# Kernel optimization log

Hardware: AMD Instinct MI355X
Metric: run time of the kernel (lower is better)

The kernel has to match this reference:

```python
import jax, jax.numpy as jnp
import numpy as np

B, T, N, K1, H, C = 2, 8, 5000, 17, 4, 16  # K1 = self + 16 neighbors
N_OUT = (C + 1) // 2


def setup_inputs() -> dict:
    key = jax.random.key(0)
    kf, kn, km = jax.random.split(key, 3)
    # small scale so exp(-||Mdf||^2) stays in a numerically interesting range
    features = jax.random.normal(kf, (B, T, N, H, C), dtype=jnp.float32) * 0.1
    nearest = jax.random.randint(kn, (N, K1), 0, N, dtype=jnp.int32)
    nearest = nearest.at[:, 0].set(jnp.arange(N, dtype=jnp.int32))  # col 0 = self
    drop = (jax.random.uniform(km, (N, K1)) < 0.05) & (jnp.arange(K1)[None, :] > 0)
    nearest = jnp.where(drop, jnp.int32(-1), nearest)
    # faithful parameter init: [I | 0] blocks scaled by Q1_init / Q2_init, diag(M_init)
    q_form = jnp.zeros((H, N_OUT, C), dtype=jnp.float32).at[:, :, :N_OUT].set(jnp.eye(N_OUT, dtype=jnp.float32))
    multiQ1 = q_form * 1.2
    multiQ2 = q_form * 0.8
    multiM = jnp.broadcast_to(jnp.eye(C, dtype=jnp.float32), (H, C, C)) * 1.5
    return {"features": features, "nearest_nodes": nearest,
            "multiQ1": multiQ1, "multiQ2": multiQ2, "multiM": multiM}


def reference(features, nearest_nodes, multiQ1, multiQ2, multiM):
    B_, T_, N_, H_, C_ = features.shape
    # pad row N_ is all-zeros; -1 sentinel indices are routed to it
    pad = jnp.concatenate([features, jnp.zeros_like(features[:, :, :1])], axis=2)  # (B,T,N+1,H,C)
    idx = jnp.where(nearest_nodes < 0, N_, nearest_nodes)  # (N, K1)

    # ---------------- undirected ----------------
    nbr = idx[:, 1:]                       # (N, K) neighbor indices (excl. self)
    fj = pad[:, :, nbr]                    # (B,T,N,K,H,C) gathered neighbor feats
    df = features[:, :, :, None] - fj      # (B,T,N,K,H,C)
    Mdf = jnp.einsum('hij,btnkhj->btnkhi', multiM, df)
    w = jnp.exp(-jnp.sum(Mdf * Mdf, axis=-1))              # (B,T,N,K,H)
    valid = (nearest_nodes[:, 1:] >= 0)[None, None, :, :, None]
    w = w * valid
    deg = jnp.sum(w, axis=3)                               # (B,T,N,H)
    pad_deg = jnp.concatenate([deg, jnp.zeros_like(deg[:, :, :1])], axis=2)
    deg_j = pad_deg[:, :, nbr]                             # (B,T,N,K,H)
    dmul = jnp.sqrt(deg[:, :, :, None] * deg_j)
    inv = jnp.where(dmul > 0, 1.0 / jnp.where(dmul > 0, dmul, 1.0), 0.0)
    u_w = w * inv                                          # (B,T,N,K,H)

    # ---------------- directed ----------------
    fi = pad[:, :-1, idx]                                  # (B,T-1,N,K1,H,C)
    Qi = jnp.einsum('hij,btnkhj->btnkhi', multiQ1, fi)     # (B,T-1,N,K1,H,n_out)
    Qj = jnp.einsum('hij,btnhj->btnhi', multiQ2, features[:, 1:])  # (B,T-1,N,H,n_out)
    wd = jnp.exp(-jnp.sum(Qi * Qj[:, :, :, None], axis=-1))        # (B,T-1,N,K1,H)
    wd = wd * (nearest_nodes >= 0)[None, None, :, :, None]
    in_deg = jnp.sum(wd, axis=3)                           # (B,T-1,N,H)
    inv_d = jnp.where(in_deg > 0, 1.0 / jnp.where(in_deg > 0, in_deg, 1.0), 0.0)
    d_w = wd * inv_d[:, :, :, None]                        # (B,T-1,N,K1,H)

    return (u_w, d_w)
```

## Files before the change

kernel.cpp:

```cpp
#include <hip/hip_runtime.h>
#include <cstdio>

#define BB 2
#define TT 8
#define NNODE 5000
#define KK1 17
#define HH 4
#define NT (BB*TT*NNODE)
#define NREST (BB*7*NNODE)
#define DEG_BLOCKS 10000
#define DW_BLOCKS 1094

typedef unsigned short u16;
typedef unsigned int u32;

__device__ __forceinline__ u16 f2bf(float x) {
  u32 u = __float_as_uint(x);
  u32 r = (u + 0x7fffu + ((u >> 16) & 1u)) >> 16;
  return (u16)r;
}
__device__ __forceinline__ float bfLo(u32 w){ return __uint_as_float(w << 16); }
__device__ __forceinline__ float bfHi(u32 w){ return __uint_as_float(w & 0xffff0000u); }

__device__ __forceinline__ float edge_e(uint4 A0, uint4 A1, uint4 B0, uint4 B1) {
  u32 aw[8] = {A0.x,A0.y,A0.z,A0.w,A1.x,A1.y,A1.z,A1.w};
  u32 bw[8] = {B0.x,B0.y,B0.z,B0.w,B1.x,B1.y,B1.z,B1.w};
  float dot = 0.f, si = 0.f, sj = 0.f;
#pragma unroll
  for (int r = 0; r < 8; ++r) {
    float al = bfLo(aw[r]), ah = bfHi(aw[r]);
    float bl = bfLo(bw[r]), bh = bfHi(bw[r]);
    dot = fmaf(al, bl, dot); dot = fmaf(ah, bh, dot);
    si  = fmaf(al, al, si);  si  = fmaf(ah, ah, si);
    sj  = fmaf(bl, bl, sj);  sj  = fmaf(bh, bh, sj);
  }
  return si + sj - 2.f*dot;
}

__global__ void __launch_bounds__(256) k_prep(
    const float* __restrict__ feat, const float* __restrict__ mm,
    const float* __restrict__ q1, const float* __restrict__ q2,
    u16* __restrict__ g, u16* __restrict__ a8, u16* __restrict__ b8) {
  const int lane = threadIdx.x & 63;
  const int h = lane >> 4, i = lane & 15;
  const int bid = blockIdx.x;
  const int x = bid & 7;
  const int local = (bid >> 3) * 4 + (threadIdx.x >> 6);
  const int mbase = x * 10000 + local * 10;
  float Mrow[16], Qrow[16];
  const float* qsrc = (i < 8) ? (q1 + (h*8 + i)*16) : (q2 + (h*8 + (i - 8))*16);
#pragma unroll
  for (int j = 0; j < 16; ++j) {
    Mrow[j] = mm[(h*16 + i)*16 + j];
    Qrow[j] = qsrc[j];
  }
#pragma unroll 2
  for (int l = 0; l < 10; ++l) {
    const int m = mbase + l;
    const float4* fp = reinterpret_cast<const float4*>(feat + (size_t)m*64 + h*16);
    float fv[16];
#pragma unroll
    for (int q = 0; q < 4; ++q) {
      float4 v = fp[q];
      fv[q*4+0] = v.x; fv[q*4+1] = v.y; fv[q*4+2] = v.z; fv[q*4+3] = v.w;
    }
    float accG = 0.f, accQ = 0.f;
#pragma unroll
    for (int j = 0; j < 16; ++j) {
      accG = fmaf(Mrow[j], fv[j], accG);
      accQ = fmaf(Qrow[j], fv[j], accQ);
    }
    g[(size_t)m*64 + lane] = f2bf(accG);
    if (i < 8) a8[(size_t)m*32 + h*8 + i] = f2bf(accQ);
    else       b8[(size_t)m*32 + h*8 + (i - 8)] = f2bf(accQ);
  }
}

__global__ void __launch_bounds__(256) k_degdw(
    const u16* __restrict__ g, const u16* __restrict__ a8, const u16* __restrict__ b8,
    const int* __restrict__ nn, float* __restrict__ deg,
    u16* __restrict__ wstage, float* __restrict__ dw) {
  __shared__ float lds[64*68];
  const int bid = blockIdx.x;
  if (bid < DEG_BLOCKS) {
    const int x = bid & 7;
    const int n = (bid >> 3)*4 + (threadIdx.x >> 6);
    const int lane = threadIdx.x & 63;
    const int k = lane >> 2, h = lane & 3;
    const int m0 = (2*x)*NNODE + n;
    const int m1 = m0 + NNODE;
    int jr = nn[n*KK1 + 1 + k];
    bool v = jr >= 0;
    int j = v ? jr : 0;
    const uint4* pi0 = reinterpret_cast<const uint4*>(g + (size_t)m0*64 + h*16);
    const uint4* pi1 = reinterpret_cast<const uint4*>(g + (size_t)m1*64 + h*16);
    const uint4* pj0 = reinterpret_cast<const uint4*>(g + (size_t)((2*x)*NNODE + j)*64 + h*16);
    const uint4* pj1 = reinterpret_cast<const uint4*>(g + (size_t)((2*x+1)*NNODE + j)*64 + h*16);
    uint4 A00 = pi0[0], A01 = pi0[1];
    uint4 A10 = pi1[0], A11 = pi1[1];
    uint4 B00 = pj0[0], B01 = pj0[1];
    uint4 B10 = pj1[0], B11 = pj1[1];
    float e0 = edge_e(A00, A01, B00, B01);
    float e1 = edge_e(A10, A11, B10, B11);
    float w0 = v ? __expf(-e0) : 0.f;
    float w1 = v ? __expf(-e1) : 0.f;
    const int soff = ((lane >> 3) << 4) + (lane & 7);
    wstage[(size_t)m0*128 + soff] = f2bf(w0);
    wstage[(size_t)m1*128 + soff] = f2bf(w1);
    float d0 = w0, d1 = w1;
    d0 += __shfl_xor(d0, 4);  d1 += __shfl_xor(d1, 4);
    d0 += __shfl_xor(d0, 8);  d1 += __shfl_xor(d1, 8);
    d0 += __shfl_xor(d0, 16); d1 += __shfl_xor(d1, 16);
    d0 += __shfl_xor(d0, 32); d1 += __shfl_xor(d1, 32);
    if (lane < 4) {
      deg[m0*4 + lane] = d0;
      deg[m1*4 + lane] = d1;
    }
  } else {
    const int wg = bid - DEG_BLOCKS;
    const int lr = threadIdx.x >> 2;
    const int h  = threadIdx.x & 3;
    const int lane = threadIdx.x & 63;
    const int qbase = lane & ~3;
    const int rest = wg*64 + lr;
    if (rest < NREST) {
      const int n = rest % NNODE;
      const int q2 = rest / NNODE;
      const int b = q2 / 7, t = q2 % 7;
      uint4 Bv = *reinterpret_cast<const uint4*>(b8 + ((size_t)((b*TT + t + 1)*NNODE + n))*32 + h*8);
      float bv[8] = {bfLo(Bv.x), bfHi(Bv.x), bfLo(Bv.y), bfHi(Bv.y),
                     bfLo(Bv.z), bfHi(Bv.z), bfLo(Bv.w), bfHi(Bv.w)};
      const int nbase = n*KK1;
      const int abase = (b*TT + t)*NNODE;
      int jvec[4];
      jvec[0] = nn[nbase + h + 0];
      jvec[1] = nn[nbase + h + 4];
      jvec[2] = nn[nbase + h + 8];
      jvec[3] = nn[nbase + h + 12];
      int j16 = nn[nbase + 16];
      float wk[17];
      float indeg = 0.f;
#pragma unroll
      for (int kk = 0; kk < 16; ++kk) {
        int jr = __shfl(jvec[kk >> 2], qbase + (kk & 3));
        bool valid = jr >= 0;
        int j = valid ? jr : 0;
        uint4 Av = *reinterpret_cast<const uint4*>(a8 + ((size_t)(abase + j))*32 + h*8);
        float dot = 0.f;
        dot = fmaf(bfLo(Av.x), bv[0], dot); dot = fmaf(bfHi(Av.x), bv[1], dot);
        dot = fmaf(bfLo(Av.y), bv[2], dot); dot = fmaf(bfHi(Av.y), bv[3], dot);
        dot = fmaf(bfLo(Av.z), bv[4], dot); dot = fmaf(bfHi(Av.z), bv[5], dot);
        dot = fmaf(bfLo(Av.w), bv[6], dot); dot = fmaf(bfHi(Av.w), bv[7], dot);
        float w = valid ? __expf(-dot) : 0.f;
        wk[kk] = w;
        indeg += w;
      }
      {
        bool valid = j16 >= 0;
        int j = valid ? j16 : 0;
        uint4 Av = *reinterpret_cast<const uint4*>(a8 + ((size_t)(abase + j))*32 + h*8);
        float dot = 0.f;
        dot = fmaf(bfLo(Av.x), bv[0], dot); dot = fmaf(bfHi(Av.x), bv[1], dot);
        dot = fmaf(bfLo(Av.y), bv[2], dot); dot = fmaf(bfHi(Av.y), bv[3], dot);
        dot = fmaf(bfLo(Av.z), bv[4], dot); dot = fmaf(bfHi(Av.z), bv[5], dot);
        dot = fmaf(bfLo(Av.w), bv[6], dot); dot = fmaf(bfHi(Av.w), bv[7], dot);
        float w = valid ? __expf(-dot) : 0.f;
        wk[16] = w;
        indeg += w;
      }
      float inv = (indeg > 0.f) ? (1.0f / indeg) : 0.f;
#pragma unroll
      for (int kk = 0; kk < KK1; ++kk) lds[lr*68 + kk*4 + h] = wk[kk] * inv;
    }
    __syncthreads();
    const int rows = NREST - wg*64;
    const int nchunks = (rows >= 64 ? 64 : rows) * 17;
    float4* obase = reinterpret_cast<float4*>(dw + (size_t)wg*4352);
    for (int c = threadIdx.x; c < nchunks; c += 256) {
      const int row = c / 17;
      const int col = (c % 17) * 4;
      obase[c] = *reinterpret_cast<const float4*>(&lds[row*68 + col]);
    }
  }
}

__global__ void __launch_bounds__(256) k_uw(
    const int* __restrict__ nn, const float* __restrict__ deg,
    float* __restrict__ uw) {
  const int bid = blockIdx.x;
  const int x = bid & 7, sub = bid >> 3;
  const int wg = (x < 4 ? x*313 : 4*313 + (x-4)*312) + sub;
  const int idx8 = (wg * 256 + threadIdx.x) * 8;
  const int m = idx8 >> 6;
  const int r8 = idx8 & 63;
  const int k0 = r8 >> 2;
  const int n = m % NNODE;
  const int btb = m - n;
  uint4 wv = *reinterpret_cast<const uint4*>(uw + idx8);
  int jr0 = nn[n*KK1 + 1 + k0];
  int jr1 = nn[n*KK1 + 2 + k0];
  float4 di = *reinterpret_cast<const float4*>(deg + (size_t)m*4);
  uint4 o0 = {0u,0u,0u,0u}, o1 = {0u,0u,0u,0u};
  if (jr0 >= 0) {
    float4 dj = *reinterpret_cast<const float4*>(deg + (size_t)(btb + jr0)*4);
    float w0 = bfLo(wv.x), w1 = bfHi(wv.x), w2 = bfLo(wv.y), w3 = bfHi(wv.y);
    float p0 = di.x*dj.x, p1 = di.y*dj.y, p2 = di.z*dj.z, p3 = di.w*dj.w;
    o0.x = __float_as_uint((w0 > 0.f && p0 > 0.f) ? w0 * rsqrtf(p0) : 0.f);
    o0.y = __float_as_uint((w1 > 0.f && p1 > 0.f) ? w1 * rsqrtf(p1) : 0.f);
    o0.z = __float_as_uint((w2 > 0.f && p2 > 0.f) ? w2 * rsqrtf(p2) : 0.f);
    o0.w = __float_as_uint((w3 > 0.f && p3 > 0.f) ? w3 * rsqrtf(p3) : 0.f);
  }
  if (jr1 >= 0) {
    float4 dj = *reinterpret_cast<const float4*>(deg + (size_t)(btb + jr1)*4);
    float w0 = bfLo(wv.z), w1 = bfHi(wv.z), w2 = bfLo(wv.w), w3 = bfHi(wv.w);
    float p0 = di.x*dj.x, p1 = di.y*dj.y, p2 = di.z*dj.z, p3 = di.w*dj.w;
    o1.x = __float_as_uint((w0 > 0.f && p0 > 0.f) ? w0 * rsqrtf(p0) : 0.f);
    o1.y = __float_as_uint((w1 > 0.f && p1 > 0.f) ? w1 * rsqrtf(p1) : 0.f);
    o1.z = __float_as_uint((w2 > 0.f && p2 > 0.f) ? w2 * rsqrtf(p2) : 0.f);
    o1.w = __float_as_uint((w3 > 0.f && p3 > 0.f) ? w3 * rsqrtf(p3) : 0.f);
  }
  uint4* ob = reinterpret_cast<uint4*>(uw + idx8);
  ob[0] = o0;
  ob[1] = o1;
}

extern "C" void kernel_launch(void* const* d_in, const int* in_sizes, int n_in,
                              void* d_out, int out_size, void* d_ws, size_t ws_size,
                              hipStream_t stream) {
  const float* feat = (const float*)d_in[0];
  const int*   nn   = (const int*)d_in[1];
  const float* q1   = (const float*)d_in[2];
  const float* q2   = (const float*)d_in[3];
  const float* mm   = (const float*)d_in[4];
  float* uw = (float*)d_out;
  float* dw = uw + (size_t)NT*64;

  const size_t G_BYTES  = (size_t)NT*64*2;
  const size_t A_BYTES  = (size_t)NT*32*2;
  const size_t DEG_BYTES= (size_t)NT*4*4;
  const size_t NEED = G_BYTES + 2*A_BYTES + DEG_BYTES;
  if (ws_size < NEED) {
    fprintf(stderr, "kernel_launch: ws_size %zu < needed %zu\n", ws_size, NEED);
    return;
  }
  u16*   g   = (u16*)d_ws;
  u16*   a8  = (u16*)((char*)d_ws + G_BYTES);
  u16*   b8  = (u16*)((char*)d_ws + G_BYTES + A_BYTES);
  float* deg = (float*)((char*)d_ws + G_BYTES + 2*A_BYTES);
  u16*   wstage = (u16*)uw;

  k_prep <<<2000, 256, 0, stream>>>(feat, mm, q1, q2, g, a8, b8);
  k_degdw<<<DEG_BLOCKS + DW_BLOCKS, 256, 0, stream>>>(g, a8, b8, nn, deg, wstage, dw);
  k_uw   <<<2500, 256, 0, stream>>>(nn, deg, uw);
}
```

Before: 62.19 us.

## Stage per-slice projected features in LDS for undirected edge weights

The projected features are re-laid out per (b,t,h) slice, and each slice (5000 nodes x 16 bf16) is loaded into 160KB of swizzled LDS. The neighbor gathers for the undirected weights then read from LDS instead of global memory. A transposed neighbor table is built in the prep kernel. The u_w normalization kernel loads the slice's degrees into LDS. The directed path is split into its own kernel, giving four launches instead of three. In exchange, each slice is reloaded by 4 blocks, only 256 blocks run with one block per CU because of the LDS size, and an extra weight staging buffer goes through global memory.

Measured after the change: 78.81 us. 1.27x slower.

```diff
diff --git a/kernel.cpp b/kernel.cpp
--- a/kernel.cpp
+++ b/kernel.cpp
@@ -1,52 +1,41 @@
 #include <hip/hip_runtime.h>
 #include <cstdio>
 
-#define BB 2
-#define TT 8
 #define NNODE 5000
 #define KK1 17
-#define HH 4
-#define NT (BB*TT*NNODE)
-#define NREST (BB*7*NNODE)
-#define DEG_BLOCKS 10000
-#define DW_BLOCKS 1094
+#define NT 80000
+#define NREST 70000
 
 typedef unsigned short u16;
 typedef unsigned int u32;
 
 __device__ __forceinline__ u16 f2bf(float x) {
   u32 u = __float_as_uint(x);
-  u32 r = (u + 0x7fffu + ((u >> 16) & 1u)) >> 16;
-  return (u16)r;
+  return (u16)((u + 0x7fffu + ((u >> 16) & 1u)) >> 16);
 }
 __device__ __forceinline__ float bfLo(u32 w){ return __uint_as_float(w << 16); }
 __device__ __forceinline__ float bfHi(u32 w){ return __uint_as_float(w & 0xffff0000u); }
-
-__device__ __forceinline__ float edge_e(uint4 A0, uint4 A1, uint4 B0, uint4 B1) {
-  u32 aw[8] = {A0.x,A0.y,A0.z,A0.w,A1.x,A1.y,A1.z,A1.w};
-  u32 bw[8] = {B0.x,B0.y,B0.z,B0.w,B1.x,B1.y,B1.z,B1.w};
-  float dot = 0.f, si = 0.f, sj = 0.f;
-#pragma unroll
-  for (int r = 0; r < 8; ++r) {
-    float al = bfLo(aw[r]), ah = bfHi(aw[r]);
-    float bl = bfLo(bw[r]), bh = bfHi(bw[r]);
-    dot = fmaf(al, bl, dot); dot = fmaf(ah, bh, dot);
-    si  = fmaf(al, al, si);  si  = fmaf(ah, ah, si);
-    sj  = fmaf(bl, bl, sj);  sj  = fmaf(bh, bh, sj);
-  }
-  return si + sj - 2.f*dot;
-}
 
 __global__ void __launch_bounds__(256) k_prep(
     const float* __restrict__ feat, const float* __restrict__ mm,
     const float* __restrict__ q1, const float* __restrict__ q2,
-    u16* __restrict__ g, u16* __restrict__ a8, u16* __restrict__ b8) {
+    const int* __restrict__ nn,
+    u16* __restrict__ gS, u16* __restrict__ a8, u16* __restrict__ b8,
+    int* __restrict__ nnT) {
+  const int bid = blockIdx.x;
+  if (bid >= 2000) {
+    const int i = (bid - 2000)*256 + threadIdx.x;
+    if (i < KK1*NNODE) {
+      const int k = i / NNODE;
+      const int n = i - k*NNODE;
+      nnT[i] = nn[n*KK1 + k];
+    }
+    return;
+  }
   const int lane = threadIdx.x & 63;
   const int h = lane >> 4, i = lane & 15;
-  const int bid = blockIdx.x;
   const int x = bid & 7;
-  const int local = (bid >> 3) * 4 + (threadIdx.x >> 6);
-  const int mbase = x * 10000 + local * 10;
+  const int mbase = x*10000 + (bid >> 3)*40 + (threadIdx.x >> 6);
   float Mrow[16], Qrow[16];
   const float* qsrc = (i < 8) ? (q1 + (h*8 + i)*16) : (q2 + (h*8 + (i - 8))*16);
 #pragma unroll
@@ -56,7 +45,9 @@
   }
 #pragma unroll 2
   for (int l = 0; l < 10; ++l) {
-    const int m = mbase + l;
+    const int m = mbase + l*4;
+    const int bt = m / NNODE;
+    const int n = m - bt*NNODE;
     const float4* fp = reinterpret_cast<const float4*>(feat + (size_t)m*64 + h*16);
     float fv[16];
 #pragma unroll
@@ -70,158 +61,181 @@
       accG = fmaf(Mrow[j], fv[j], accG);
       accQ = fmaf(Qrow[j], fv[j], accQ);
     }
-    g[(size_t)m*64 + lane] = f2bf(accG);
+    gS[((size_t)(bt*4 + h)*NNODE + n)*16 + i] = f2bf(accG);
     if (i < 8) a8[(size_t)m*32 + h*8 + i] = f2bf(accQ);
     else       b8[(size_t)m*32 + h*8 + (i - 8)] = f2bf(accQ);
   }
 }
 
-__global__ void __launch_bounds__(256) k_degdw(
-    const u16* __restrict__ g, const u16* __restrict__ a8, const u16* __restrict__ b8,
-    const int* __restrict__ nn, float* __restrict__ deg,
-    u16* __restrict__ wstage, float* __restrict__ dw) {
+__global__ void __launch_bounds__(256) k_w(
+    const u16* __restrict__ gS, const int* __restrict__ nnT,
+    float* __restrict__ degS, u16* __restrict__ wS) {
+  __shared__ u32 glds[40000];
+  const int bid = blockIdx.x;
+  const int sl = bid & 63;
+  const int chunk = bid >> 6;
+  const u32* gsrc = reinterpret_cast<const u32*>(gS) + (size_t)sl*NNODE*8;
+  for (int n = threadIdx.x; n < NNODE; n += 256) {
+    const uint4* rp = reinterpret_cast<const uint4*>(gsrc + n*8);
+    uint4 v0 = rp[0], v1 = rp[1];
+    u32 wv[8] = {v0.x, v0.y, v0.z, v0.w, v1.x, v1.y, v1.z, v1.w};
+    const int sw = (n >> 2) & 7;
+#pragma unroll
+    for (int c = 0; c < 8; ++c) glds[n*8 + (c ^ sw)] = wv[c];
+  }
+  __syncthreads();
+  for (int r = 0; r < 5; ++r) {
+    const int ns = r*256 + threadIdx.x;
+    if (ns >= 1250) continue;
+    const int n = chunk*1250 + ns;
+    float av[16];
+    float si = 0.f;
+    const int swn = (n >> 2) & 7;
+#pragma unroll
+    for (int c = 0; c < 8; ++c) {
+      u32 wv = glds[n*8 + (c ^ swn)];
+      float lo = bfLo(wv), hi = bfHi(wv);
+      av[2*c] = lo; av[2*c+1] = hi;
+      si = fmaf(lo, lo, si); si = fmaf(hi, hi, si);
+    }
+    float deg = 0.f;
+    u32 packed[8];
+#pragma unroll 4
+    for (int k = 0; k < 16; ++k) {
+      const int jr = nnT[(1 + k)*NNODE + n];
+      const int j = (jr >= 0) ? jr : 0;
+      const int swj = (j >> 2) & 7;
+      float dot = 0.f, sj = 0.f;
+#pragma unroll
+      for (int c = 0; c < 8; ++c) {
+        u32 wv = glds[j*8 + (c ^ swj)];
+        float lo = bfLo(wv), hi = bfHi(wv);
+        dot = fmaf(av[2*c], lo, dot); dot = fmaf(av[2*c+1], hi, dot);
+        sj = fmaf(lo, lo, sj); sj = fmaf(hi, hi, sj);
+      }
+      float e = si + sj - 2.f*dot;
+      float w = (jr >= 0) ? __expf(-e) : 0.f;
+      deg += w;
+      u16 wb = f2bf(w);
+      if (k & 1) packed[k >> 1] |= ((u32)wb) << 16;
+      else       packed[k >> 1] = (u32)wb;
+    }
+    degS[(size_t)sl*NNODE + n] = deg;
+    uint4* wp = reinterpret_cast<uint4*>(wS + ((size_t)sl*NNODE + n)*16);
+    wp[0] = make_uint4(packed[0], packed[1], packed[2], packed[3]);
+    wp[1] = make_uint4(packed[4], packed[5], packed[6], packed[7]);
+  }
+}
+
+__global__ void __launch_bounds__(256) k_uw3(
+    const u16* __restrict__ wS, const int* __restrict__ nnT,
+    const float* __restrict__ degS, float* __restrict__ uw) {
+  __shared__ float dl[4*NNODE];
+  const int bid = blockIdx.x;
+  const int bt = bid & 15;
+  const int chunk = bid >> 4;
+  for (int i = threadIdx.x; i < 4*NNODE; i += 256) dl[i] = degS[(size_t)bt*4*NNODE + i];
+  __syncthreads();
+  const u32* wsrc = reinterpret_cast<const u32*>(wS);
+  for (int r = 0; r < 10; ++r) {
+    const int item = r*256 + threadIdx.x;
+    const int nsub = item >> 3, kp = item & 7;
+    const int n = chunk*313 + nsub;
+    if (nsub >= 313 || n >= NNODE) continue;
+    const int j0r = nnT[(1 + 2*kp)*NNODE + n];
+    const int j1r = nnT[(2 + 2*kp)*NNODE + n];
+    const int j0 = (j0r >= 0) ? j0r : 0;
+    const int j1 = (j1r >= 0) ? j1r : 0;
+    u32 wv[4];
+#pragma unroll
+    for (int h = 0; h < 4; ++h) wv[h] = wsrc[((size_t)(bt*4 + h)*NNODE + n)*8 + kp];
+    float o0[4], o1[4];
+#pragma unroll
+    for (int h = 0; h < 4; ++h) {
+      const float di  = dl[h*NNODE + n];
+      const float dj0 = dl[h*NNODE + j0];
+      const float dj1 = dl[h*NNODE + j1];
+      const float w0 = bfLo(wv[h]), w1 = bfHi(wv[h]);
+      const float p0 = di*dj0, p1 = di*dj1;
+      o0[h] = (j0r >= 0 && w0 > 0.f && p0 > 0.f) ? w0*rsqrtf(p0) : 0.f;
+      o1[h] = (j1r >= 0 && w1 > 0.f && p1 > 0.f) ? w1*rsqrtf(p1) : 0.f;
+    }
+    float4* ob = reinterpret_cast<float4*>(uw + (((size_t)bt*NNODE + n)*16 + 2*kp)*4);
+    ob[0] = make_float4(o0[0], o0[1], o0[2], o0[3]);
+    ob[1] = make_float4(o1[0], o1[1], o1[2], o1[3]);
+  }
+}
+
+__global__ void __launch_bounds__(256) k_dw(
+    const u16* __restrict__ a8, const u16* __restrict__ b8,
+    const int* __restrict__ nn, float* __restrict__ dw) {
   __shared__ float lds[64*68];
   const int bid = blockIdx.x;
-  if (bid < DEG_BLOCKS) {
-    const int x = bid & 7;
-    const int n = (bid >> 3)*4 + (threadIdx.x >> 6);
-    const int lane = threadIdx.x & 63;
-    const int k = lane >> 2, h = lane & 3;
-    const int m0 = (2*x)*NNODE + n;
-    const int m1 = m0 + NNODE;
-    int jr = nn[n*KK1 + 1 + k];
-    bool v = jr >= 0;
-    int j = v ? jr : 0;
-    const uint4* pi0 = reinterpret_cast<const uint4*>(g + (size_t)m0*64 + h*16);
-    const uint4* pi1 = reinterpret_cast<const uint4*>(g + (size_t)m1*64 + h*16);
-    const uint4* pj0 = reinterpret_cast<const uint4*>(g + (size_t)((2*x)*NNODE + j)*64 + h*16);
-    const uint4* pj1 = reinterpret_cast<const uint4*>(g + (size_t)((2*x+1)*NNODE + j)*64 + h*16);
-    uint4 A00 = pi0[0], A01 = pi0[1];
-    uint4 A10 = pi1[0], A11 = pi1[1];
-    uint4 B00 = pj0[0], B01 = pj0[1];
-    uint4 B10 = pj1[0], B11 = pj1[1];
-    float e0 = edge_e(A00, A01, B00, B01);
-    float e1 = edge_e(A10, A11, B10, B11);
-    float w0 = v ? __expf(-e0) : 0.f;
-    float w1 = v ? __expf(-e1) : 0.f;
-    const int soff = ((lane >> 3) << 4) + (lane & 7);
-    wstage[(size_t)m0*128 + soff] = f2bf(w0);
-    wstage[(size_t)m1*128 + soff] = f2bf(w1);
-    float d0 = w0, d1 = w1;
-    d0 += __shfl_xor(d0, 4);  d1 += __shfl_xor(d1, 4);
-    d0 += __shfl_xor(d0, 8);  d1 += __shfl_xor(d1, 8);
-    d0 += __shfl_xor(d0, 16); d1 += __shfl_xor(d1, 16);
-    d0 += __shfl_xor(d0, 32); d1 += __shfl_xor(d1, 32);
-    if (lane < 4) {
-      deg[m0*4 + lane] = d0;
-      deg[m1*4 + lane] = d1;
-    }
-  } else {
-    const int wg = bid - DEG_BLOCKS;
-    const int lr = threadIdx.x >> 2;
-    const int h  = threadIdx.x & 3;
-    const int lane = threadIdx.x & 63;
-    const int qbase = lane & ~3;
-    const int rest = wg*64 + lr;
-    if (rest < NREST) {
-      const int n = rest % NNODE;
-      const int q2 = rest / NNODE;
-      const int b = q2 / 7, t = q2 % 7;
-      uint4 Bv = *reinterpret_cast<const uint4*>(b8 + ((size_t)((b*TT + t + 1)*NNODE + n))*32 + h*8);
-      float bv[8] = {bfLo(Bv.x), bfHi(Bv.x), bfLo(Bv.y), bfHi(Bv.y),
-                     bfLo(Bv.z), bfHi(Bv.z), bfLo(Bv.w), bfHi(Bv.w)};
-      const int nbase = n*KK1;
-      const int abase = (b*TT + t)*NNODE;
-      int jvec[4];
-      jvec[0] = nn[nbase + h + 0];
-      jvec[1] = nn[nbase + h + 4];
-      jvec[2] = nn[nbase + h + 8];
-      jvec[3] = nn[nbase + h + 12];
-      int j16 = nn[nbase + 16];
-      float wk[17];
-      float indeg = 0.f;
-#pragma unroll
-      for (int kk = 0; kk < 16; ++kk) {
-        int jr = __shfl(jvec[kk >> 2], qbase + (kk & 3));
-        bool valid = jr >= 0;
-        int j = valid ? jr : 0;
-        uint4 Av = *reinterpret_cast<const uint4*>(a8 + ((size_t)(abase + j))*32 + h*8);
-        float dot = 0.f;
-        dot = fmaf(bfLo(Av.x), bv[0], dot); dot = fmaf(bfHi(Av.x), bv[1], dot);
-        dot = fmaf(bfLo(Av.y), bv[2], dot); dot = fmaf(bfHi(Av.y), bv[3], dot);
-        dot = fmaf(bfLo(Av.z), bv[4], dot); dot = fmaf(bfHi(Av.z), bv[5], dot);
-        dot = fmaf(bfLo(Av.w), bv[6], dot); dot = fmaf(bfHi(Av.w), bv[7], dot);
-        float w = valid ? __expf(-dot) : 0.f;
-        wk[kk] = w;
-        indeg += w;
-      }
-      {
-        bool valid = j16 >= 0;
-        int j = valid ? j16 : 0;
-        uint4 Av = *reinterpret_cast<const uint4*>(a8 + ((size_t)(abase + j))*32 + h*8);
-        float dot = 0.f;
-        dot = fmaf(bfLo(Av.x), bv[0], dot); dot = fmaf(bfHi(Av.x), bv[1], dot);
-        dot = fmaf(bfLo(Av.y), bv[2], dot); dot = fmaf(bfHi(Av.y), bv[3], dot);
-        dot = fmaf(bfLo(Av.z), bv[4], dot); dot = fmaf(bfHi(Av.z), bv[5], dot);
-        dot = fmaf(bfLo(Av.w), bv[6], dot); dot = fmaf(bfHi(Av.w), bv[7], dot);
-        float w = valid ? __expf(-dot) : 0.f;
-        wk[16] = w;
-        indeg += w;
-      }
-      float inv = (indeg > 0.f) ? (1.0f / indeg) : 0.f;
-#pragma unroll
-      for (int kk = 0; kk < KK1; ++kk) lds[lr*68 + kk*4 + h] = wk[kk] * inv;
-    }
-    __syncthreads();
-    const int rows = NREST - wg*64;
-    const int nchunks = (rows >= 64 ? 64 : rows) * 17;
-    float4* obase = reinterpret_cast<float4*>(dw + (size_t)wg*4352);
-    for (int c = threadIdx.x; c < nchunks; c += 256) {
-      const int row = c / 17;
-      const int col = (c % 17) * 4;
-      obase[c] = *reinterpret_cast<const float4*>(&lds[row*68 + col]);
-    }
-  }
-}
-
-__global__ void __launch_bounds__(256) k_uw(
-    const int* __restrict__ nn, const float* __restrict__ deg,
-    float* __restrict__ uw) {
-  const int bid = blockIdx.x;
   const int x = bid & 7, sub = bid >> 3;
-  const int wg = (x < 4 ? x*313 : 4*313 + (x-4)*312) + sub;
-  const int idx8 = (wg * 256 + threadIdx.x) * 8;
-  const int m = idx8 >> 6;
-  const int r8 = idx8 & 63;
-  const int k0 = r8 >> 2;
-  const int n = m % NNODE;
-  const int btb = m - n;
-  uint4 wv = *reinterpret_cast<const uint4*>(uw + idx8);
-  int jr0 = nn[n*KK1 + 1 + k0];
-  int jr1 = nn[n*KK1 + 2 + k0];
-  float4 di = *reinterpret_cast<const float4*>(deg + (size_t)m*4);
-  uint4 o0 = {0u,0u,0u,0u}, o1 = {0u,0u,0u,0u};
-  if (jr0 >= 0) {
-    float4 dj = *reinterpret_cast<const float4*>(deg + (size_t)(btb + jr0)*4);
-    float w0 = bfLo(wv.x), w1 = bfHi(wv.x), w2 = bfLo(wv.y), w3 = bfHi(wv.y);
-    float p0 = di.x*dj.x, p1 = di.y*dj.y, p2 = di.z*dj.z, p3 = di.w*dj.w;
-    o0.x = __float_as_uint((w0 > 0.f && p0 > 0.f) ? w0 * rsqrtf(p0) : 0.f);
-    o0.y = __float_as_uint((w1 > 0.f && p1 > 0.f) ? w1 * rsqrtf(p1) : 0.f);
-    o0.z = __float_as_uint((w2 > 0.f && p2 > 0.f) ? w2 * rsqrtf(p2) : 0.f);
-    o0.w = __float_as_uint((w3 > 0.f && p3 > 0.f) ? w3 * rsqrtf(p3) : 0.f);
-  }
-  if (jr1 >= 0) {
-    float4 dj = *reinterpret_cast<const float4*>(deg + (size_t)(btb + jr1)*4);
-    float w0 = bfLo(wv.z), w1 = bfHi(wv.z), w2 = bfLo(wv.w), w3 = bfHi(wv.w);
-    float p0 = di.x*dj.x, p1 = di.y*dj.y, p2 = di.z*dj.z, p3 = di.w*dj.w;
-    o1.x = __float_as_uint((w0 > 0.f && p0 > 0.f) ? w0 * rsqrtf(p0) : 0.f);
-    o1.y = __float_as_uint((w1 > 0.f && p1 > 0.f) ? w1 * rsqrtf(p1) : 0.f);
-    o1.z = __float_as_uint((w2 > 0.f && p2 > 0.f) ? w2 * rsqrtf(p2) : 0.f);
-    o1.w = __float_as_uint((w3 > 0.f && p3 > 0.f) ? w3 * rsqrtf(p3) : 0.f);
-  }
-  uint4* ob = reinterpret_cast<uint4*>(uw + idx8);
-  ob[0] = o0;
-  ob[1] = o1;
+  const int wg = (x < 6 ? x*137 : 6*137 + (x-6)*136) + sub;
+  const int lr = threadIdx.x >> 2;
+  const int h  = threadIdx.x & 3;
+  const int lane = threadIdx.x & 63;
+  const int qbase = lane & ~3;
+  const int rest = wg*64 + lr;
+  if (rest < NREST) {
+    const int n = rest % NNODE;
+    const int q2 = rest / NNODE;
+    const int b = q2 / 7, t = q2 % 7;
+    uint4 Bv = *reinterpret_cast<const uint4*>(b8 + ((size_t)((b*8 + t + 1)*NNODE + n))*32 + h*8);
+    float bv[8] = {bfLo(Bv.x), bfHi(Bv.x), bfLo(Bv.y), bfHi(Bv.y),
+                   bfLo(Bv.z), bfHi(Bv.z), bfLo(Bv.w), bfHi(Bv.w)};
+    const int nbase = n*KK1;
+    const int abase = (b*8 + t)*NNODE;
+    int jvec[4];
+    jvec[0] = nn[nbase + h + 0];
+    jvec[1] = nn[nbase + h + 4];
+    jvec[2] = nn[nbase + h + 8];
+    jvec[3] = nn[nbase + h + 12];
+    int j16 = nn[nbase + 16];
+    float wk[17];
+    float indeg = 0.f;
+#pragma unroll
+    for (int kk = 0; kk < 16; ++kk) {
+      int jr = __shfl(jvec[kk >> 2], qbase + (kk & 3));
+      bool valid = jr >= 0;
+      int j = valid ? jr : 0;
+      uint4 Av = *reinterpret_cast<const uint4*>(a8 + ((size_t)(abase + j))*32 + h*8);
+      float dot = 0.f;
+      dot = fmaf(bfLo(Av.x), bv[0], dot); dot = fmaf(bfHi(Av.x), bv[1], dot);
+      dot = fmaf(bfLo(Av.y), bv[2], dot); dot = fmaf(bfHi(Av.y), bv[3], dot);
+      dot = fmaf(bfLo(Av.z), bv[4], dot); dot = fmaf(bfHi(Av.z), bv[5], dot);
+      dot = fmaf(bfLo(Av.w), bv[6], dot); dot = fmaf(bfHi(Av.w), bv[7], dot);
+      float w = valid ? __expf(-dot) : 0.f;
+      wk[kk] = w;
+      indeg += w;
+    }
+    {
+      bool valid = j16 >= 0;
+      int j = valid ? j16 : 0;
+      uint4 Av = *reinterpret_cast<const uint4*>(a8 + ((size_t)(abase + j))*32 + h*8);
+      float dot = 0.f;
+      dot = fmaf(bfLo(Av.x), bv[0], dot); dot = fmaf(bfHi(Av.x), bv[1], dot);
+      dot = fmaf(bfLo(Av.y), bv[2], dot); dot = fmaf(bfHi(Av.y), bv[3], dot);
+      dot = fmaf(bfLo(Av.z), bv[4], dot); dot = fmaf(bfHi(Av.z), bv[5], dot);
+      dot = fmaf(bfLo(Av.w), bv[6], dot); dot = fmaf(bfHi(Av.w), bv[7], dot);
+      float w = valid ? __expf(-dot) : 0.f;
+      wk[16] = w;
+      indeg += w;
+    }
+    float inv = (indeg > 0.f) ? (1.0f / indeg) : 0.f;
+#pragma unroll
+    for (int kk = 0; kk < KK1; ++kk) lds[lr*68 + kk*4 + h] = wk[kk] * inv;
+  }
+  __syncthreads();
+  const int rows = NREST - wg*64;
+  const int nchunks = (rows >= 64 ? 64 : rows) * 17;
+  float4* obase = reinterpret_cast<float4*>(dw + (size_t)wg*4352);
+  for (int c = threadIdx.x; c < nchunks; c += 256) {
+    const int row = c / 17;
+    const int col = (c % 17) * 4;
+    obase[c] = *reinterpret_cast<const float4*>(&lds[row*68 + col]);
+  }
 }
 
 extern "C" void kernel_launch(void* const* d_in, const int* in_sizes, int n_in,
@@ -235,21 +249,25 @@
   float* uw = (float*)d_out;
   float* dw = uw + (size_t)NT*64;
 
-  const size_t G_BYTES  = (size_t)NT*64*2;
+  const size_t GS_BYTES = (size_t)NT*64*2;
   const size_t A_BYTES  = (size_t)NT*32*2;
-  const size_t DEG_BYTES= (size_t)NT*4*4;
-  const size_t NEED = G_BYTES + 2*A_BYTES + DEG_BYTES;
+  const size_t DEG_BYTES= (size_t)64*NNODE*4;
+  const size_t W_BYTES  = (size_t)64*NNODE*16*2;
+  const size_t NNT_BYTES= (size_t)KK1*NNODE*4;
+  const size_t NEED = GS_BYTES + 2*A_BYTES + DEG_BYTES + W_BYTES + NNT_BYTES;
   if (ws_size < NEED) {
     fprintf(stderr, "kernel_launch: ws_size %zu < needed %zu\n", ws_size, NEED);
     return;
   }
-  u16*   g   = (u16*)d_ws;
-  u16*   a8  = (u16*)((char*)d_ws + G_BYTES);
-  u16*   b8  = (u16*)((char*)d_ws + G_BYTES + A_BYTES);
-  float* deg = (float*)((char*)d_ws + G_BYTES + 2*A_BYTES);
-  u16*   wstage = (u16*)uw;
-
-  k_prep <<<2000, 256, 0, stream>>>(feat, mm, q1, q2, g, a8, b8);
-  k_degdw<<<DEG_BLOCKS + DW_BLOCKS, 256, 0, stream>>>(g, a8, b8, nn, deg, wstage, dw);
-  k_uw   <<<2500, 256, 0, stream>>>(nn, deg, uw);
-}
+  u16*   gS   = (u16*)d_ws;
+  u16*   a8   = (u16*)((char*)d_ws + GS_BYTES);
+  u16*   b8   = (u16*)((char*)d_ws + GS_BYTES + A_BYTES);
+  float* degS = (float*)((char*)d_ws + GS_BYTES + 2*A_BYTES);
+  u16*   wS   = (u16*)((char*)d_ws + GS_BYTES + 2*A_BYTES + DEG_BYTES);
+  int*   nnT  = (int*)((char*)d_ws + GS_BYTES + 2*A_BYTES + DEG_BYTES + W_BYTES);
+
+  k_prep<<<2333, 256, 0, stream>>>(feat, mm, q1, q2, nn, gS, a8, b8, nnT);
+  k_w   <<<256, 256, 0, stream>>>(gS, nnT, degS, wS);
+  k_uw3 <<<256, 256, 0, stream>>>(wS, nnT, degS, uw);
+  k_dw  <<<1094, 256, 0, stream>>>(a8, b8, nn, dw);
+}
```

## Fuse prep, degree/directed and normalize stages into one cooperative persistent kernel

Applied to the files above, without the earlier changes.

Replaces the three launches with a single cooperative kernel of 512 persistent blocks that runs projection, then degree plus directed weights, then undirected normalization, separated by grid-wide syncs. Undirected edge weights stay in registers across the grid sync instead of being staged as bf16 in the output buffer and reloaded, and the normalization uses rsqrtf. This removes the inter-kernel launch gaps and a global round trip. In exchange, occupancy is limited to 512 blocks with heavy per-thread register arrays, and the grid syncs add their own cost. The old three-kernel path is kept as a fallback if the cooperative launch fails.

Result: slower. 206.2 us (+231.6%).

```diff
diff --git a/kernel.cpp b/kernel.cpp
--- a/kernel.cpp
+++ b/kernel.cpp
@@ -1,23 +1,21 @@
 #include <hip/hip_runtime.h>
+#include <hip/hip_cooperative_groups.h>
 #include <cstdio>
 
-#define BB 2
-#define TT 8
+namespace cg = cooperative_groups;
+
 #define NNODE 5000
 #define KK1 17
-#define HH 4
-#define NT (BB*TT*NNODE)
-#define NREST (BB*7*NNODE)
-#define DEG_BLOCKS 10000
-#define DW_BLOCKS 1094
+#define NT 80000
+#define NREST 70000
+#define NBLK 512
 
 typedef unsigned short u16;
 typedef unsigned int u32;
 
 __device__ __forceinline__ u16 f2bf(float x) {
   u32 u = __float_as_uint(x);
-  u32 r = (u + 0x7fffu + ((u >> 16) & 1u)) >> 16;
-  return (u16)r;
+  return (u16)((u + 0x7fffu + ((u >> 16) & 1u)) >> 16);
 }
 __device__ __forceinline__ float bfLo(u32 w){ return __uint_as_float(w << 16); }
 __device__ __forceinline__ float bfHi(u32 w){ return __uint_as_float(w & 0xffff0000u); }
@@ -37,7 +35,188 @@
   return si + sj - 2.f*dot;
 }
 
-__global__ void __launch_bounds__(256) k_prep(
+__device__ __forceinline__ void dw_block(
+    const u16* __restrict__ a8, const u16* __restrict__ b8,
+    const int* __restrict__ nn, float* __restrict__ dw,
+    float* lds, int v, int tid) {
+  const int xx = v & 7, sub = v >> 3;
+  const int wg = (xx < 6 ? xx*137 : 6*137 + (xx-6)*136) + sub;
+  const int lr = tid >> 2;
+  const int hd = tid & 3;
+  const int lane = tid & 63;
+  const int qbase = lane & ~3;
+  const int rest = wg*64 + lr;
+  if (rest < NREST) {
+    const int n = rest % NNODE;
+    const int q2i = rest / NNODE;
+    const int b = q2i / 7, t = q2i % 7;
+    uint4 Bv = *reinterpret_cast<const uint4*>(b8 + ((size_t)((b*8 + t + 1)*NNODE + n))*32 + hd*8);
+    float bv[8] = {bfLo(Bv.x), bfHi(Bv.x), bfLo(Bv.y), bfHi(Bv.y),
+                   bfLo(Bv.z), bfHi(Bv.z), bfLo(Bv.w), bfHi(Bv.w)};
+    const int nbase = n*KK1;
+    const int abase = (b*8 + t)*NNODE;
+    int jvec[4];
+    jvec[0] = nn[nbase + hd + 0];
+    jvec[1] = nn[nbase + hd + 4];
+    jvec[2] = nn[nbase + hd + 8];
+    jvec[3] = nn[nbase + hd + 12];
+    int j16 = nn[nbase + 16];
+    float wk[17];
+    float indeg = 0.f;
+#pragma unroll
+    for (int kk = 0; kk < 16; ++kk) {
+      int jr = __shfl(jvec[kk >> 2], qbase + (kk & 3));
+      bool valid = jr >= 0;
+      int j = valid ? jr : 0;
+      uint4 Av = *reinterpret_cast<const uint4*>(a8 + ((size_t)(abase + j))*32 + hd*8);
+      float dot = 0.f;
+      dot = fmaf(bfLo(Av.x), bv[0], dot); dot = fmaf(bfHi(Av.x), bv[1], dot);
+      dot = fmaf(bfLo(Av.y), bv[2], dot); dot = fmaf(bfHi(Av.y), bv[3], dot);
+      dot = fmaf(bfLo(Av.z), bv[4], dot); dot = fmaf(bfHi(Av.z), bv[5], dot);
+      dot = fmaf(bfLo(Av.w), bv[6], dot); dot = fmaf(bfHi(Av.w), bv[7], dot);
+      float w = valid ? __expf(-dot) : 0.f;
+      wk[kk] = w;
+      indeg += w;
+    }
+    {
+      bool valid = j16 >= 0;
+      int j = valid ? j16 : 0;
+      uint4 Av = *reinterpret_cast<const uint4*>(a8 + ((size_t)(abase + j))*32 + hd*8);
+      float dot = 0.f;
+      dot = fmaf(bfLo(Av.x), bv[0], dot); dot = fmaf(bfHi(Av.x), bv[1], dot);
+      dot = fmaf(bfLo(Av.y), bv[2], dot); dot = fmaf(bfHi(Av.y), bv[3], dot);
+      dot = fmaf(bfLo(Av.z), bv[4], dot); dot = fmaf(bfHi(Av.z), bv[5], dot);
+      dot = fmaf(bfLo(Av.w), bv[6], dot); dot = fmaf(bfHi(Av.w), bv[7], dot);
+      float w = valid ? __expf(-dot) : 0.f;
+      wk[16] = w;
+      indeg += w;
+    }
+    float inv = (indeg > 0.f) ? (1.0f / indeg) : 0.f;
+#pragma unroll
+    for (int kk = 0; kk < KK1; ++kk) lds[lr*68 + kk*4 + hd] = wk[kk] * inv;
+  }
+  __syncthreads();
+  const int rows = NREST - wg*64;
+  const int nchunks = (rows >= 64 ? 64 : rows) * 17;
+  float4* obase = reinterpret_cast<float4*>(dw + (size_t)wg*4352);
+  for (int c = tid; c < nchunks; c += 256) {
+    const int row = c / 17;
+    const int col = (c % 17) * 4;
+    obase[c] = *reinterpret_cast<const float4*>(&lds[row*68 + col]);
+  }
+  __syncthreads();
+}
+
+__global__ void __launch_bounds__(256, 2) k_fused(
+    const float* __restrict__ feat, const float* __restrict__ mm,
+    const float* __restrict__ q1, const float* __restrict__ q2,
+    const int* __restrict__ nn,
+    u16* __restrict__ g, u16* __restrict__ a8, u16* __restrict__ b8,
+    float* __restrict__ deg, float* __restrict__ uw, float* __restrict__ dw) {
+  __shared__ float lds[64*68];
+  cg::grid_group gg = cg::this_grid();
+  const int bid = blockIdx.x;
+  const int tid = threadIdx.x;
+  const int lane = tid & 63;
+  const int wid = tid >> 6;
+
+  {
+    const int h = lane >> 4, i = lane & 15;
+    const int gw = bid*4 + wid;
+    float Mrow[16], Qrow[16];
+    const float* qsrc = (i < 8) ? (q1 + (h*8 + i)*16) : (q2 + (h*8 + (i - 8))*16);
+#pragma unroll
+    for (int j = 0; j < 16; ++j) {
+      Mrow[j] = mm[(h*16 + i)*16 + j];
+      Qrow[j] = qsrc[j];
+    }
+    for (int it = 0; it < 40; ++it) {
+      const int m = it*2048 + gw;
+      if (m >= NT) break;
+      const float4* fp = reinterpret_cast<const float4*>(feat + (size_t)m*64 + h*16);
+      float fv[16];
+#pragma unroll
+      for (int q = 0; q < 4; ++q) {
+        float4 v = fp[q];
+        fv[q*4+0] = v.x; fv[q*4+1] = v.y; fv[q*4+2] = v.z; fv[q*4+3] = v.w;
+      }
+      float accG = 0.f, accQ = 0.f;
+#pragma unroll
+      for (int j = 0; j < 16; ++j) {
+        accG = fmaf(Mrow[j], fv[j], accG);
+        accQ = fmaf(Qrow[j], fv[j], accQ);
+      }
+      g[(size_t)m*64 + lane] = f2bf(accG);
+      if (i < 8) a8[(size_t)m*32 + h*8 + i] = f2bf(accQ);
+      else       b8[(size_t)m*32 + h*8 + (i - 8)] = f2bf(accQ);
+    }
+  }
+  gg.sync();
+
+  const int x = bid & 7;
+  const int lw = (bid >> 3)*4 + wid;
+  const int kq = lane >> 2, hh = lane & 3;
+  float wreg0[20], wreg1[20];
+#pragma unroll
+  for (int it = 0; it < 20; ++it) {
+    const int n = it*256 + lw;
+    wreg0[it] = 0.f; wreg1[it] = 0.f;
+    if (n < NNODE) {
+      const int m0 = (2*x)*NNODE + n, m1 = m0 + NNODE;
+      int jr = nn[n*KK1 + 1 + kq];
+      bool v = jr >= 0;
+      int j = v ? jr : 0;
+      const uint4* pi0 = reinterpret_cast<const uint4*>(g + (size_t)m0*64 + hh*16);
+      const uint4* pi1 = reinterpret_cast<const uint4*>(g + (size_t)m1*64 + hh*16);
+      const uint4* pj0 = reinterpret_cast<const uint4*>(g + (size_t)((2*x)*NNODE + j)*64 + hh*16);
+      const uint4* pj1 = reinterpret_cast<const uint4*>(g + (size_t)((2*x+1)*NNODE + j)*64 + hh*16);
+      uint4 A00 = pi0[0], A01 = pi0[1];
+      uint4 A10 = pi1[0], A11 = pi1[1];
+      uint4 B00 = pj0[0], B01 = pj0[1];
+      uint4 B10 = pj1[0], B11 = pj1[1];
+      float e0 = edge_e(A00, A01, B00, B01);
+      float e1 = edge_e(A10, A11, B10, B11);
+      float w0 = v ? __expf(-e0) : 0.f;
+      float w1 = v ? __expf(-e1) : 0.f;
+      wreg0[it] = w0; wreg1[it] = w1;
+      float d0 = w0, d1 = w1;
+      d0 += __shfl_xor(d0, 4);  d1 += __shfl_xor(d1, 4);
+      d0 += __shfl_xor(d0, 8);  d1 += __shfl_xor(d1, 8);
+      d0 += __shfl_xor(d0, 16); d1 += __shfl_xor(d1, 16);
+      d0 += __shfl_xor(d0, 32); d1 += __shfl_xor(d1, 32);
+      if (lane < 4) {
+        deg[m0*4 + lane] = d0;
+        deg[m1*4 + lane] = d1;
+      }
+    }
+  }
+
+  for (int itv = 0; itv < 3; ++itv) {
+    const int v = itv*NBLK + bid;
+    if (v < 1094) dw_block(a8, b8, nn, dw, lds, v, tid);
+  }
+  gg.sync();
+
+#pragma unroll
+  for (int it = 0; it < 20; ++it) {
+    const int n = it*256 + lw;
+    if (n >= NNODE) continue;
+    const int m0 = (2*x)*NNODE + n, m1 = m0 + NNODE;
+    int jr = nn[n*KK1 + 1 + kq];
+    bool v = jr >= 0;
+    int j = v ? jr : 0;
+    float di0 = deg[m0*4 + hh];
+    float di1 = deg[m1*4 + hh];
+    float dj0 = deg[((2*x)*NNODE + j)*4 + hh];
+    float dj1 = deg[((2*x+1)*NNODE + j)*4 + hh];
+    float w0 = wreg0[it], w1 = wreg1[it];
+    float p0 = di0*dj0, p1 = di1*dj1;
+    uw[(size_t)m0*64 + lane] = (v && w0 > 0.f && p0 > 0.f) ? w0 * rsqrtf(p0) : 0.f;
+    uw[(size_t)m1*64 + lane] = (v && w1 > 0.f && p1 > 0.f) ? w1 * rsqrtf(p1) : 0.f;
+  }
+}
+
+__global__ void __launch_bounds__(256) k_prep_f(
     const float* __restrict__ feat, const float* __restrict__ mm,
     const float* __restrict__ q1, const float* __restrict__ q2,
     u16* __restrict__ g, u16* __restrict__ a8, u16* __restrict__ b8) {
@@ -76,26 +255,27 @@
   }
 }
 
-__global__ void __launch_bounds__(256) k_degdw(
+__global__ void __launch_bounds__(256) k_degdw_f(
     const u16* __restrict__ g, const u16* __restrict__ a8, const u16* __restrict__ b8,
     const int* __restrict__ nn, float* __restrict__ deg,
     u16* __restrict__ wstage, float* __restrict__ dw) {
   __shared__ float lds[64*68];
   const int bid = blockIdx.x;
-  if (bid < DEG_BLOCKS) {
+  if (bid < 10000) {
     const int x = bid & 7;
     const int n = (bid >> 3)*4 + (threadIdx.x >> 6);
     const int lane = threadIdx.x & 63;
-    const int k = lane >> 2, h = lane & 3;
+    const int hh = lane & 3;
+    const int kq = lane >> 2;
     const int m0 = (2*x)*NNODE + n;
     const int m1 = m0 + NNODE;
-    int jr = nn[n*KK1 + 1 + k];
+    int jr = nn[n*KK1 + 1 + kq];
     bool v = jr >= 0;
     int j = v ? jr : 0;
-    const uint4* pi0 = reinterpret_cast<const uint4*>(g + (size_t)m0*64 + h*16);
-    const uint4* pi1 = reinterpret_cast<const uint4*>(g + (size_t)m1*64 + h*16);
-    const uint4* pj0 = reinterpret_cast<const uint4*>(g + (size_t)((2*x)*NNODE + j)*64 + h*16);
-    const uint4* pj1 = reinterpret_cast<const uint4*>(g + (size_t)((2*x+1)*NNODE + j)*64 + h*16);
+    const uint4* pi0 = reinterpret_cast<const uint4*>(g + (size_t)m0*64 + hh*16);
+    const uint4* pi1 = reinterpret_cast<const uint4*>(g + (size_t)m1*64 + hh*16);
+    const uint4* pj0 = reinterpret_cast<const uint4*>(g + (size_t)((2*x)*NNODE + j)*64 + hh*16);
+    const uint4* pj1 = reinterpret_cast<const uint4*>(g + (size_t)((2*x+1)*NNODE + j)*64 + hh*16);
     uint4 A00 = pi0[0], A01 = pi0[1];
     uint4 A10 = pi1[0], A11 = pi1[1];
     uint4 B00 = pj0[0], B01 = pj0[1];
@@ -117,74 +297,11 @@
       deg[m1*4 + lane] = d1;
     }
   } else {
-    const int wg = bid - DEG_BLOCKS;
-    const int lr = threadIdx.x >> 2;
-    const int h  = threadIdx.x & 3;
-    const int lane = threadIdx.x & 63;
-    const int qbase = lane & ~3;
-    const int rest = wg*64 + lr;
-    if (rest < NREST) {
-      const int n = rest % NNODE;
-      const int q2 = rest / NNODE;
-      const int b = q2 / 7, t = q2 % 7;
-      uint4 Bv = *reinterpret_cast<const uint4*>(b8 + ((size_t)((b*TT + t + 1)*NNODE + n))*32 + h*8);
-      float bv[8] = {bfLo(Bv.x), bfHi(Bv.x), bfLo(Bv.y), bfHi(Bv.y),
-                     bfLo(Bv.z), bfHi(Bv.z), bfLo(Bv.w), bfHi(Bv.w)};
-      const int nbase = n*KK1;
-      const int abase = (b*TT + t)*NNODE;
-      int jvec[4];
-      jvec[0] = nn[nbase + h + 0];
-      jvec[1] = nn[nbase + h + 4];
-      jvec[2] = nn[nbase + h + 8];
-      jvec[3] = nn[nbase + h + 12];
-      int j16 = nn[nbase + 16];
-      float wk[17];
-      float indeg = 0.f;
-#pragma unroll
-      for (int kk = 0; kk < 16; ++kk) {
-        int jr = __shfl(jvec[kk >> 2], qbase + (kk & 3));
-        bool valid = jr >= 0;
-        int j = valid ? jr : 0;
-        uint4 Av = *reinterpret_cast<const uint4*>(a8 + ((size_t)(abase + j))*32 + h*8);
-        float dot = 0.f;
-        dot = fmaf(bfLo(Av.x), bv[0], dot); dot = fmaf(bfHi(Av.x), bv[1], dot);
-        dot = fmaf(bfLo(Av.y), bv[2], dot); dot = fmaf(bfHi(Av.y), bv[3], dot);
-        dot = fmaf(bfLo(Av.z), bv[4], dot); dot = fmaf(bfHi(Av.z), bv[5], dot);
-        dot = fmaf(bfLo(Av.w), bv[6], dot); dot = fmaf(bfHi(Av.w), bv[7], dot);
-        float w = valid ? __expf(-dot) : 0.f;
-        wk[kk] = w;
-        indeg += w;
-      }
-      {
-        bool valid = j16 >= 0;
-        int j = valid ? j16 : 0;
-        uint4 Av = *reinterpret_cast<const uint4*>(a8 + ((size_t)(abase + j))*32 + h*8);
-        float dot = 0.f;
-        dot = fmaf(bfLo(Av.x), bv[0], dot); dot = fmaf(bfHi(Av.x), bv[1], dot);
-        dot = fmaf(bfLo(Av.y), bv[2], dot); dot = fmaf(bfHi(Av.y), bv[3], dot);
-        dot = fmaf(bfLo(Av.z), bv[4], dot); dot = fmaf(bfHi(Av.z), bv[5], dot);
-        dot = fmaf(bfLo(Av.w), bv[6], dot); dot = fmaf(bfHi(Av.w), bv[7], dot);
-        float w = valid ? __expf(-dot) : 0.f;
-        wk[16] = w;
-        indeg += w;
-      }
-      float inv = (indeg > 0.f) ? (1.0f / indeg) : 0.f;
-#pragma unroll
-      for (int kk = 0; kk < KK1; ++kk) lds[lr*68 + kk*4 + h] = wk[kk] * inv;
-    }
-    __syncthreads();
-    const int rows = NREST - wg*64;
-    const int nchunks = (rows >= 64 ? 64 : rows) * 17;
-    float4* obase = reinterpret_cast<float4*>(dw + (size_t)wg*4352);
-    for (int c = threadIdx.x; c < nchunks; c += 256) {
-      const int row = c / 17;
-      const int col = (c % 17) * 4;
-      obase[c] = *reinterpret_cast<const float4*>(&lds[row*68 + col]);
-    }
-  }
-}
-
-__global__ void __launch_bounds__(256) k_uw(
+    dw_block(a8, b8, nn, dw, lds, bid - 10000, threadIdx.x);
+  }
+}
+
+__global__ void __launch_bounds__(256) k_uw_f(
     const int* __restrict__ nn, const float* __restrict__ deg,
     float* __restrict__ uw) {
   const int bid = blockIdx.x;
@@ -247,9 +364,18 @@
   u16*   a8  = (u16*)((char*)d_ws + G_BYTES);
   u16*   b8  = (u16*)((char*)d_ws + G_BYTES + A_BYTES);
   float* deg = (float*)((char*)d_ws + G_BYTES + 2*A_BYTES);
-  u16*   wstage = (u16*)uw;
-
-  k_prep <<<2000, 256, 0, stream>>>(feat, mm, q1, q2, g, a8, b8);
-  k_degdw<<<DEG_BLOCKS + DW_BLOCKS, 256, 0, stream>>>(g, a8, b8, nn, deg, wstage, dw);
-  k_uw   <<<2500, 256, 0, stream>>>(nn, deg, uw);
-}
+
+  void* args[] = {(void*)&feat, (void*)&mm, (void*)&q1, (void*)&q2, (void*)&nn,
+                  (void*)&g, (void*)&a8, (void*)&b8, (void*)&deg,
+                  (void*)&uw, (void*)&dw};
+  hipError_t err = hipLaunchCooperativeKernel((const void*)k_fused, dim3(NBLK),
+                                              dim3(256), args, 0, stream);
+  if (err != hipSuccess) {
+    fprintf(stderr, "coop launch failed (%d: %s) -> fallback path\n",
+            (int)err, hipGetErrorString(err));
+    u16* wstage = (u16*)uw;
+    k_prep_f <<<2000, 256, 0, stream>>>(feat, mm, q1, q2, g, a8, b8);
+    k_degdw_f<<<11094, 256, 0, stream>>>(g, a8, b8, nn, deg, wstage, dw);
+    k_uw_f   <<<2500, 256, 0, stream>>>(nn, deg, uw);
+  }
+}
```
